# Kernel tuning notes

Measured on AMD Instinct MI355X. Metric: run time of the kernel, lower is better.

## Reference

```python
import jax, jax.numpy as jnp
import numpy as np

B, L, DW, DP = 128, 512, 256, 64
NF = 512          # num_filters == types == nr (forced by U.view / maxpool in source)
D = DW + 2 * DP   # 384
DWIN = 3 * D      # windowed feature width


def setup_inputs() -> dict:
    key = jax.random.key(0)
    ks = jax.random.split(key, 10)
    return {
        "x": jax.random.normal(ks[0], (B, L, DW), jnp.float32),
        "e1": jax.random.normal(ks[1], (B, DW), jnp.float32),
        "e2": jax.random.normal(ks[2], (B, DW), jnp.float32),
        "posVec": jax.random.normal(ks[3], (B, L, 2 * DP), jnp.float32),
        "We1": jax.random.normal(ks[4], (DW, DW), jnp.float32),
        "We2": jax.random.normal(ks[5], (DW, DW), jnp.float32),
        "U": jax.random.normal(ks[6], (NF, NF), jnp.float32),
        "conv_w": jax.random.normal(ks[7], (NF, DWIN), jnp.float32) * 0.02,
        "conv_b": jnp.zeros((NF,), jnp.float32),
        "rel_w": jax.random.normal(ks[8], (NF, NF), jnp.float32) * 0.02,  # y_embedding.weight (nr, num_filters)
    }


def reference(x, e1, e2, posVec, We1, We2, U, conv_w, conv_b, rel_w):
    # ---- input attention ----
    x_concat = jnp.concatenate([x, posVec], axis=-1)            # (B, L, D)
    px = jnp.pad(x_concat, ((0, 0), (1, 1), (0, 0)))            # pad seq by k=1
    w_concat = jnp.concatenate(
        [px[:, 0:L], px[:, 1:L + 1], px[:, 2:L + 2]], axis=-1)  # (B, L, 3D)
    A1 = jnp.einsum('bld,de,be->bl', x, We1, e1)                # (B, L)
    A2 = jnp.einsum('bld,de,be->bl', x, We2, e2)
    alpha = 0.5 * (jax.nn.softmax(A1, axis=1) + jax.nn.softmax(A2, axis=1))
    R = w_concat * alpha[:, :, None]                            # (B, L, 3D)
    # ---- convolution (kernel spans full window -> per-position linear) ----
    conv = jnp.tanh(jnp.einsum('bld,fd->bfl', R, conv_w) + conv_b[None, :, None])  # (B, F, L)
    # ---- attentive pooling ----
    G = jnp.einsum('bfl,ft,rt->blr', conv, U, rel_w)            # (B, L, nr)
    AP = jax.nn.softmax(G, axis=1)                              # softmax over seq positions
    wo = jnp.einsum('bfl,blr->bfr', conv, AP)                   # (B, F, nr)
    wo = jnp.max(wo, axis=2)                                    # MaxPool2d((1, types)) -> (B, F)
    wo = jax.nn.relu(wo)
    return wo, rel_w
```

## Files before the change

kernel.cpp:

```cpp
#include <hip/hip_runtime.h>
#include <hip/hip_bf16.h>

#define BB 128
#define LL 512
#define DW 256
#define DP 64
#define NF 512
#define DD 384
#define DWIN 1152
#define RR 512
#define LP 514

typedef __attribute__((ext_vector_type(8))) short short8;
typedef __attribute__((ext_vector_type(4))) short short4v;
typedef __attribute__((ext_vector_type(2))) short short2v;
typedef __attribute__((ext_vector_type(8))) _Float16 half8;
typedef __attribute__((ext_vector_type(4))) float f32x4;
typedef __attribute__((ext_vector_type(2))) float f32x2;

typedef __attribute__((address_space(1))) const void* gas_t;
typedef __attribute__((address_space(3))) void* las_t;

__device__ __forceinline__ void stage16(const void* g, void* l) {
    __builtin_amdgcn_global_load_lds((gas_t)g, (las_t)l, 16, 0, 0);
}

__device__ inline short f2h(float v) {
    _Float16 h = (_Float16)v;
    return *reinterpret_cast<short*>(&h);
}
__device__ inline int xcd_swz(int bid, int nwg) {
    return (bid & 7) * (nwg >> 3) + (bid >> 3);
}

__global__ void k_ve(const float* __restrict__ We1, const float* __restrict__ We2,
                     const float* __restrict__ e1, const float* __restrict__ e2,
                     float* __restrict__ v1, float* __restrict__ v2) {
    int b = blockIdx.x;
    int d = threadIdx.x;
    __shared__ float s1[DW], s2[DW];
    s1[d] = e1[b * DW + d];
    s2[d] = e2[b * DW + d];
    __syncthreads();
    float a1 = 0.f, a2 = 0.f;
    for (int e = 0; e < DW; ++e) {
        a1 += We1[d * DW + e] * s1[e];
        a2 += We2[d * DW + e] * s2[e];
    }
    v1[b * DW + d] = a1;
    v2[b * DW + d] = a2;
}

__global__ __launch_bounds__(256) void k_pack_logits(
    const float* __restrict__ x, const float* __restrict__ pv,
    const float* __restrict__ v1, const float* __restrict__ v2,
    short* __restrict__ pxp, float* __restrict__ A1, float* __restrict__ A2) {
    int gr = blockIdx.x * 4 + (threadIdx.x >> 6);
    int lane = threadIdx.x & 63;
    int b = gr / LP;
    int rr = gr - b * LP;
    short* dst = pxp + (size_t)gr * DD;
    if (rr == 0 || rr == LP - 1) {
        *(short4v*)(dst + lane * 4) = (short4v){0, 0, 0, 0};
        *(short2v*)(dst + 256 + lane * 2) = (short2v){0, 0};
        return;
    }
    int l = rr - 1;
    f32x4 xv = *(const f32x4*)(x + ((size_t)b * LL + l) * DW + lane * 4);
    f32x2 pvv = *(const f32x2*)(pv + ((size_t)b * LL + l) * (2 * DP) + lane * 2);
    f32x4 w1 = *(const f32x4*)(v1 + b * DW + lane * 4);
    f32x4 w2 = *(const f32x4*)(v2 + b * DW + lane * 4);
    float p1 = xv[0] * w1[0] + xv[1] * w1[1] + xv[2] * w1[2] + xv[3] * w1[3];
    float p2 = xv[0] * w2[0] + xv[1] * w2[1] + xv[2] * w2[2] + xv[3] * w2[3];
    for (int off = 32; off; off >>= 1) {
        p1 += __shfl_down(p1, off);
        p2 += __shfl_down(p2, off);
    }
    short4v ox;
#pragma unroll
    for (int j = 0; j < 4; ++j) ox[j] = f2h(xv[j]);
    *(short4v*)(dst + lane * 4) = ox;
    short2v op;
    op[0] = f2h(pvv[0]);
    op[1] = f2h(pvv[1]);
    *(short2v*)(dst + 256 + lane * 2) = op;
    if (lane == 0) { A1[b * LL + l] = p1; A2[b * LL + l] = p2; }
}

__global__ void k_alpha(const float* __restrict__ A1, const float* __restrict__ A2,
                        float* __restrict__ alpha) {
    int b = blockIdx.x;
    int l = threadIdx.x;
    __shared__ float s[LL];
    float a1 = A1[b * LL + l], a2 = A2[b * LL + l];

    s[l] = a1; __syncthreads();
    for (int st = 256; st; st >>= 1) { if (l < st) s[l] = fmaxf(s[l], s[l + st]); __syncthreads(); }
    float m1 = s[0]; __syncthreads();
    float e1x = expf(a1 - m1);
    s[l] = e1x; __syncthreads();
    for (int st = 256; st; st >>= 1) { if (l < st) s[l] += s[l + st]; __syncthreads(); }
    float d1 = s[0]; __syncthreads();

    s[l] = a2; __syncthreads();
    for (int st = 256; st; st >>= 1) { if (l < st) s[l] = fmaxf(s[l], s[l + st]); __syncthreads(); }
    float m2 = s[0]; __syncthreads();
    float e2x = expf(a2 - m2);
    s[l] = e2x; __syncthreads();
    for (int st = 256; st; st >>= 1) { if (l < st) s[l] += s[l + st]; __syncthreads(); }
    float d2 = s[0];

    alpha[b * LL + l] = 0.5f * (e1x / d1 + e2x / d2);
}

__global__ __launch_bounds__(256) void k_pack_w(const float* __restrict__ cw,
                                                short* __restrict__ cwb) {
    int idx = blockIdx.x * 256 + threadIdx.x;
    const float* src = cw + (size_t)idx * 8;
    f32x4 u0 = *(const f32x4*)(src);
    f32x4 u1 = *(const f32x4*)(src + 4);
    short8 v;
#pragma unroll
    for (int jj = 0; jj < 4; ++jj) { v[jj] = f2h(u0[jj]); v[jj + 4] = f2h(u1[jj]); }
    *(short8*)(cwb + (size_t)idx * 8) = v;
}

__global__ void k_w2t(const float* __restrict__ U, const float* __restrict__ relw,
                      short* __restrict__ Qf) {
    __shared__ float As[16][65], Bs[16][65];
    int r0 = blockIdx.y * 64, f0 = blockIdx.x * 64;
    int tid = threadIdx.x, ty = tid >> 4, tx = tid & 15;
    float acc[4][4] = {};
    for (int k0 = 0; k0 < NF; k0 += 16) {
        for (int i = 0; i < 4; ++i) {
            int lin = tid + 256 * i;
            int kk = lin & 15, mm = lin >> 4;
            As[kk][mm] = relw[(r0 + mm) * NF + k0 + kk];
            Bs[kk][mm] = U[(f0 + mm) * NF + k0 + kk];
        }
        __syncthreads();
        for (int kk = 0; kk < 16; ++kk) {
            float av[4], bv[4];
            for (int i = 0; i < 4; ++i) av[i] = As[kk][ty * 4 + i];
            for (int j = 0; j < 4; ++j) bv[j] = Bs[kk][tx * 4 + j];
            for (int i = 0; i < 4; ++i)
                for (int j = 0; j < 4; ++j) acc[i][j] += av[i] * bv[j];
        }
        __syncthreads();
    }
    for (int i = 0; i < 4; ++i)
        for (int j = 0; j < 4; ++j)
            Qf[(size_t)(r0 + ty * 4 + i) * NF + f0 + tx * 4 + j] = f2h(acc[i][j]);
}

__global__ __launch_bounds__(512, 2) void k_conv_mfma(
    const short* __restrict__ pxp, const short* __restrict__ cwb,
    const float* __restrict__ conv_b, const float* __restrict__ alpha,
    short* __restrict__ conv_lf, short* __restrict__ conv_fl) {
    int wg = xcd_swz(blockIdx.x, 512);
    int b = wg >> 2;
    int bl0 = ((wg >> 1) & 1) * 256;
    int bf0 = (wg & 1) * 256;
    int tid = threadIdx.x;
    int lane = tid & 63, w = tid >> 6;
    int wm = w >> 2, wn = w & 3;
    int lr = lane & 15, lg = lane >> 4;

    __shared__ __align__(16) char smem[131072];

    f32x4 acc[8][4];
#pragma unroll
    for (int i = 0; i < 8; ++i)
#pragma unroll
        for (int j = 0; j < 4; ++j) acc[i][j] = (f32x4){0.f, 0.f, 0.f, 0.f};

    int srow = lane >> 3;
    int sw = (lane & 7) ^ srow;
    const short* gA = pxp + ((size_t)b * LP + bl0 + w * 8 + srow) * DD + sw * 8;
    const short* gB = cwb + (size_t)(bf0 + w * 8 + srow) * DWIN + sw * 8;
    int p7 = lr & 7;

    {
        char* nb = smem;
#pragma unroll
        for (int c = 0; c < 4; ++c) {
            stage16(gA + (size_t)(64 * c) * DD, nb + (c * 64 + w * 8) * 128);
            stage16(gB + (size_t)(64 * c) * DWIN, nb + 32768 + (c * 64 + w * 8) * 128);
        }
    }
    __syncthreads();

    for (int kt = 0; kt < 18; ++kt) {
        const char* cb = smem + (kt & 1) * 65536;
        if (kt + 1 < 18) {
            char* nb = smem + ((kt + 1) & 1) * 65536;
            int k0 = (kt + 1) * 64;
#pragma unroll
            for (int c = 0; c < 4; ++c) {
                stage16(gA + (size_t)(64 * c) * DD + k0, nb + (c * 64 + w * 8) * 128);
                stage16(gB + (size_t)(64 * c) * DWIN + k0, nb + 32768 + (c * 64 + w * 8) * 128);
            }
        }
        half8 bf[4][2];
#pragma unroll
        for (int ni = 0; ni < 4; ++ni)
#pragma unroll
            for (int ks = 0; ks < 2; ++ks) {
                int cs = ks * 4 + lg;
                bf[ni][ks] = *(const half8*)(cb + 32768 +
                    (wn * 64 + ni * 16 + lr) * 128 + ((cs ^ p7) * 16));
            }
#pragma unroll
        for (int mh = 0; mh < 2; ++mh) {
            half8 af[4][2];
#pragma unroll
            for (int mi = 0; mi < 4; ++mi)
#pragma unroll
                for (int ks = 0; ks < 2; ++ks) {
                    int cs = ks * 4 + lg;
                    af[mi][ks] = *(const half8*)(cb +
                        (wm * 128 + mh * 64 + mi * 16 + lr) * 128 + ((cs ^ p7) * 16));
                }
            __builtin_amdgcn_s_setprio(1);
#pragma unroll
            for (int mi = 0; mi < 4; ++mi)
#pragma unroll
                for (int ni = 0; ni < 4; ++ni)
#pragma unroll
                    for (int ks = 0; ks < 2; ++ks)
                        acc[mh * 4 + mi][ni] = __builtin_amdgcn_mfma_f32_16x16x32_f16(
                            af[mi][ks], bf[ni][ks], acc[mh * 4 + mi][ni], 0, 0, 0);
            __builtin_amdgcn_s_setprio(0);
        }
        __syncthreads();
    }

    char* T = smem;
#pragma unroll
    for (int mi = 0; mi < 8; ++mi) {
        int lloc = wm * 128 + mi * 16 + lg * 4;
        int l = bl0 + lloc;
        f32x4 av = *(const f32x4*)(alpha + (size_t)b * LL + l);
#pragma unroll
        for (int ni = 0; ni < 4; ++ni) {
            int floc = wn * 64 + ni * 16 + lr;
            int f = bf0 + floc;
            float bias = conv_b[f];
            short4v o;
#pragma unroll
            for (int r = 0; r < 4; ++r) {
                float val = tanhf(av[r] * acc[mi][ni][r] + bias);
                short sv = f2h(val);
                o[r] = sv;
                conv_lf[((size_t)b * LL + l + r) * NF + f] = sv;
            }
            int c16 = lloc >> 3;
            *(short4v*)(T + floc * 512 + ((c16 ^ (floc & 31)) << 4) + (lloc & 7) * 2) = o;
        }
    }
    __syncthreads();
#pragma unroll
    for (int i = 0; i < 16; ++i) {
        int lin = tid + 512 * i;
        int frow = lin >> 5;
        int c16 = lin & 31;
        short8 v = *(const short8*)(T + frow * 512 + ((c16 ^ (frow & 31)) << 4));
        *(short8*)(conv_fl + ((size_t)b * NF + bf0 + frow) * LL + bl0 + c16 * 8) = v;
    }
}

__global__ __launch_bounds__(512) void k_g_mfma(
    const short* __restrict__ Qf,
    const short* __restrict__ convlf, _Float16* __restrict__ Gp) {
    const float LOG2E = 1.4426950408889634f;
    int wg = xcd_swz(blockIdx.x, 512);
    int b = wg >> 2;
    int r0 = (wg & 3) * 128;
    int tid = threadIdx.x, lane = tid & 63, w = tid >> 6;
    int wm = w >> 2, wn = w & 3;
    int lr = lane & 15, lg = lane >> 4;

    __shared__ __align__(16) char smem[81920];
    short* Ab = (short*)smem;
    short* Bb = (short*)(smem + 16384);
    float (*rowred)[4] = (float(*)[4])smem;

    f32x4 acc[4][8];
#pragma unroll
    for (int i = 0; i < 4; ++i)
#pragma unroll
        for (int j = 0; j < 8; ++j) acc[i][j] = (f32x4){0.f, 0.f, 0.f, 0.f};

    int trow = tid >> 3;
    int sw = (tid & 7) ^ (trow & 7);
    const short* gA = Qf + (size_t)(r0 + trow) * NF + sw * 8;
    const short* gB = convlf + (size_t)b * LL * NF + (size_t)trow * NF + sw * 8;
    short* lAd = Ab + w * 512;
    short* lBd = Bb + w * 512;
    int p7 = lr & 7;

    for (int kb = 0; kb < 8; ++kb) {
        int k0 = kb * 64;
#pragma unroll
        for (int c = 0; c < 2; ++c)
            stage16(gA + (size_t)(64 * c) * NF + k0, lAd + c * 4096);
#pragma unroll
        for (int c = 0; c < 8; ++c)
            stage16(gB + (size_t)(64 * c) * NF + k0, lBd + c * 4096);
        __syncthreads();
#pragma unroll
        for (int kk = 0; kk < 2; ++kk) {
            int cs = (kk << 2) + lg;
            half8 af[4], bf[8];
#pragma unroll
            for (int mi = 0; mi < 4; ++mi)
                af[mi] = *(const half8*)(Ab + (wm * 64 + mi * 16 + lr) * 64 + ((cs ^ p7) * 8));
#pragma unroll
            for (int ni = 0; ni < 8; ++ni)
                bf[ni] = *(const half8*)(Bb + (wn * 128 + ni * 16 + lr) * 64 + ((cs ^ p7) * 8));
#pragma unroll
            for (int mi = 0; mi < 4; ++mi)
#pragma unroll
                for (int ni = 0; ni < 8; ++ni)
                    acc[mi][ni] = __builtin_amdgcn_mfma_f32_16x16x32_f16(
                        af[mi], bf[ni], acc[mi][ni], 0, 0, 0);
        }
        __syncthreads();
    }

    float mrow[4][4];
#pragma unroll
    for (int mi = 0; mi < 4; ++mi)
#pragma unroll
        for (int rr = 0; rr < 4; ++rr) {
            float m = acc[mi][0][rr];
#pragma unroll
            for (int ni = 1; ni < 8; ++ni) m = fmaxf(m, acc[mi][ni][rr]);
            m = fmaxf(m, __shfl_xor(m, 1));
            m = fmaxf(m, __shfl_xor(m, 2));
            m = fmaxf(m, __shfl_xor(m, 4));
            m = fmaxf(m, __shfl_xor(m, 8));
            mrow[mi][rr] = m;
        }
    if (lr == 0) {
#pragma unroll
        for (int mi = 0; mi < 4; ++mi)
#pragma unroll
            for (int rr = 0; rr < 4; ++rr)
                rowred[wm * 64 + mi * 16 + lg * 4 + rr][wn] = mrow[mi][rr];
    }
    __syncthreads();
#pragma unroll
    for (int mi = 0; mi < 4; ++mi)
#pragma unroll
        for (int rr = 0; rr < 4; ++rr) {
            f32x4 rv = *(const f32x4*)rowred[wm * 64 + mi * 16 + lg * 4 + rr];
            mrow[mi][rr] = fmaxf(fmaxf(rv[0], rv[1]), fmaxf(rv[2], rv[3]));
        }
    __syncthreads();
    float srow[4][4];
#pragma unroll
    for (int mi = 0; mi < 4; ++mi)
#pragma unroll
        for (int rr = 0; rr < 4; ++rr) {
            float s = 0.f;
            float m = mrow[mi][rr];
#pragma unroll
            for (int ni = 0; ni < 8; ++ni) {
                float pp = exp2f((acc[mi][ni][rr] - m) * LOG2E);
                acc[mi][ni][rr] = pp;
                s += pp;
            }
            s += __shfl_xor(s, 1);
            s += __shfl_xor(s, 2);
            s += __shfl_xor(s, 4);
            s += __shfl_xor(s, 8);
            srow[mi][rr] = s;
        }
    if (lr == 0) {
#pragma unroll
        for (int mi = 0; mi < 4; ++mi)
#pragma unroll
            for (int rr = 0; rr < 4; ++rr)
                rowred[wm * 64 + mi * 16 + lg * 4 + rr][wn] = srow[mi][rr];
    }
    __syncthreads();
#pragma unroll
    for (int mi = 0; mi < 4; ++mi)
#pragma unroll
        for (int rr = 0; rr < 4; ++rr) {
            f32x4 rv = *(const f32x4*)rowred[wm * 64 + mi * 16 + lg * 4 + rr];
            srow[mi][rr] = 1.f / (rv[0] + rv[1] + rv[2] + rv[3]);
        }

#pragma unroll
    for (int mi = 0; mi < 4; ++mi)
#pragma unroll
        for (int ni = 0; ni < 8; ++ni)
#pragma unroll
            for (int rr = 0; rr < 4; ++rr) {
                int r = r0 + wm * 64 + mi * 16 + lg * 4 + rr;
                int l = wn * 128 + ni * 16 + lr;
                Gp[((size_t)b * RR + r) * LL + l] = (_Float16)(acc[mi][ni][rr] * srow[mi][rr]);
            }
}

__global__ __launch_bounds__(256) void k_wo_mfma(
    const short* __restrict__ convfl, const short* __restrict__ P,
    float* __restrict__ out) {
    int wg = xcd_swz(blockIdx.x, 2048);
    int b = wg >> 4;
    int f0 = ((wg >> 2) & 3) * 128;
    int r0 = (wg & 3) * 128;
    int tid = threadIdx.x, lane = tid & 63, w = tid >> 6;
    int wm = w >> 1, wn = w & 1;
    int lr = lane & 15, lg = lane >> 4;

    __shared__ __align__(16) char smem[65536];

    f32x4 acc[4][4];
    for (int i = 0; i < 4; ++i)
        for (int j = 0; j < 4; ++j) acc[i][j] = (f32x4){0.f, 0.f, 0.f, 0.f};

    int rowA = lane >> 3;
    int sw = (lane & 7) ^ rowA;
    const short* gA = convfl + (size_t)b * NF * LL + (size_t)(f0 + w * 32 + rowA) * LL + sw * 8;
    const short* gB = P + (size_t)b * RR * LL + (size_t)(r0 + w * 32 + rowA) * LL + sw * 8;
    int rA = wm * 64, rB = wn * 64;
    int p7 = lr & 7;

    {
        char* nbuf = smem;
#pragma unroll
        for (int c = 0; c < 4; ++c) {
            stage16(gA + (size_t)(8 * c) * LL, nbuf + w * 4096 + c * 1024);
            stage16(gB + (size_t)(8 * c) * LL, nbuf + 16384 + w * 4096 + c * 1024);
        }
    }

    for (int t = 0; t < 8; ++t) {
        char* cbuf = smem + (t & 1) * 32768;
        if (t + 1 < 8) {
            char* nbuf = smem + ((t + 1) & 1) * 32768;
            int k0 = (t + 1) * 64;
#pragma unroll
            for (int c = 0; c < 4; ++c) {
                stage16(gA + (size_t)(8 * c) * LL + k0, nbuf + w * 4096 + c * 1024);
                stage16(gB + (size_t)(8 * c) * LL + k0, nbuf + 16384 + w * 4096 + c * 1024);
            }
            asm volatile("s_waitcnt vmcnt(8)" ::: "memory");
        } else {
            asm volatile("s_waitcnt vmcnt(0)" ::: "memory");
        }
        __builtin_amdgcn_s_barrier();
        __builtin_amdgcn_sched_barrier(0);
        const short (*Ac)[64] = (const short(*)[64])cbuf;
        const short (*Bc)[64] = (const short(*)[64])(cbuf + 16384);
#pragma unroll
        for (int kk = 0; kk < 2; ++kk) {
            half8 af[4], bf[4];
            int cs = ((kk << 2) + lg);
#pragma unroll
            for (int mi = 0; mi < 4; ++mi)
                af[mi] = *(const half8*)(&Ac[rA + mi * 16 + lr][(cs ^ p7) * 8]);
#pragma unroll
            for (int ni = 0; ni < 4; ++ni)
                bf[ni] = *(const half8*)(&Bc[rB + ni * 16 + lr][(cs ^ p7) * 8]);
#pragma unroll
            for (int mi = 0; mi < 4; ++mi)
#pragma unroll
                for (int ni = 0; ni < 4; ++ni)
                    acc[mi][ni] = __builtin_amdgcn_mfma_f32_16x16x32_f16(
                        af[mi], bf[ni], acc[mi][ni], 0, 0, 0);
        }
        __builtin_amdgcn_sched_barrier(0);
        __builtin_amdgcn_s_barrier();
        __builtin_amdgcn_sched_barrier(0);
    }

    int fbase = f0 + wm * 64;
#pragma unroll
    for (int mi = 0; mi < 4; ++mi)
#pragma unroll
        for (int rr = 0; rr < 4; ++rr) {
            float m = acc[mi][0][rr];
#pragma unroll
            for (int ni = 1; ni < 4; ++ni) m = fmaxf(m, acc[mi][ni][rr]);
            m = fmaxf(m, __shfl_xor(m, 1));
            m = fmaxf(m, __shfl_xor(m, 2));
            m = fmaxf(m, __shfl_xor(m, 4));
            m = fmaxf(m, __shfl_xor(m, 8));
            if (lr == 0 && m > 0.f) {
                int f = fbase + mi * 16 + lg * 4 + rr;
                atomicMax((int*)&out[(size_t)b * NF + f], __float_as_int(m));
            }
        }
}

extern "C" void kernel_launch(void* const* d_in, const int* in_sizes, int n_in,
                              void* d_out, int out_size, void* d_ws, size_t ws_size,
                              hipStream_t stream) {
    const float* x      = (const float*)d_in[0];
    const float* e1     = (const float*)d_in[1];
    const float* e2     = (const float*)d_in[2];
    const float* posVec = (const float*)d_in[3];
    const float* We1    = (const float*)d_in[4];
    const float* We2    = (const float*)d_in[5];
    const float* U      = (const float*)d_in[6];
    const float* conv_w = (const float*)d_in[7];
    const float* conv_b = (const float*)d_in[8];
    const float* rel_w  = (const float*)d_in[9];
    float* out = (float*)d_out;

    char* p = (char*)d_ws;
    short* convlf = (short*)p;  p += (size_t)BB * LL * NF * 2;
    short* convfl = (short*)p;  p += (size_t)BB * NF * LL * 2;
    _Float16* Gp  = (_Float16*)p;  p += (size_t)BB * RR * LL * 2;
    short* pxp    = (short*)p;  p += (size_t)BB * LP * DD * 2;
    short* cwb    = (short*)p;  p += (size_t)NF * DWIN * 2;
    short* QfW    = (short*)p;  p += (size_t)RR * NF * 2;
    float* v1     = (float*)p;  p += (size_t)BB * DW * 4;
    float* v2     = (float*)p;  p += (size_t)BB * DW * 4;
    float* A1     = (float*)p;  p += (size_t)BB * LL * 4;
    float* A2     = (float*)p;  p += (size_t)BB * LL * 4;
    float* alpha  = (float*)p;  p += (size_t)BB * LL * 4;

    k_ve<<<BB, DW, 0, stream>>>(We1, We2, e1, e2, v1, v2);
    k_pack_logits<<<(BB * LP) / 4, 256, 0, stream>>>(x, posVec, v1, v2, pxp, A1, A2);
    k_alpha<<<BB, LL, 0, stream>>>(A1, A2, alpha);
    k_pack_w<<<(NF * DWIN / 8) / 256, 256, 0, stream>>>(conv_w, cwb);
    k_w2t<<<dim3(NF / 64, RR / 64), 256, 0, stream>>>(U, rel_w, QfW);
    k_conv_mfma<<<512, 512, 0, stream>>>(pxp, cwb, conv_b, alpha, convlf, convfl);
    k_g_mfma<<<512, 512, 0, stream>>>(QfW, convlf, Gp);
    hipMemsetAsync(d_out, 0, (size_t)BB * NF * sizeof(float), stream);
    k_wo_mfma<<<2048, 256, 0, stream>>>(convfl, (const short*)Gp, out);
    hipMemcpyAsync(out + BB * NF, rel_w, (size_t)NF * RR * sizeof(float),
                   hipMemcpyDeviceToDevice, stream);
}
```

Baseline: 315.5 us.

## Split conv GEMM K-loop into four phased sub-steps with finer-grained staging

Restructures the conv MFMA main loop into four phases per K tile. B and each half of A now have separate double buffers, and async global-to-LDS loads for the next tile are issued in chunks with explicit vmcnt waits and raw s_barrier instead of one full __syncthreads per tile. The A-row-to-wave mapping is permuted so each phase handles 32 rows per wave, and the epilogue index math is updated to match. The launch bound no longer requests two blocks per CU, which frees registers but may lower occupancy.

```diff
diff --git a/kernel.cpp b/kernel.cpp
--- a/kernel.cpp
+++ b/kernel.cpp
@@ -153,7 +153,7 @@
             Qf[(size_t)(r0 + ty * 4 + i) * NF + f0 + tx * 4 + j] = f2h(acc[i][j]);
 }
 
-__global__ __launch_bounds__(512, 2) void k_conv_mfma(
+__global__ __launch_bounds__(512) void k_conv_mfma(
     const short* __restrict__ pxp, const short* __restrict__ cwb,
     const float* __restrict__ conv_b, const float* __restrict__ alpha,
     short* __restrict__ conv_lf, short* __restrict__ conv_fl) {
@@ -174,71 +174,92 @@
 #pragma unroll
         for (int j = 0; j < 4; ++j) acc[i][j] = (f32x4){0.f, 0.f, 0.f, 0.f};
 
-    int srow = lane >> 3;
-    int sw = (lane & 7) ^ srow;
-    const short* gA = pxp + ((size_t)b * LP + bl0 + w * 8 + srow) * DD + sw * 8;
-    const short* gB = cwb + (size_t)(bf0 + w * 8 + srow) * DWIN + sw * 8;
+    int srow8 = w * 8 + (lane >> 3);
+    int swc = (lane & 7) ^ (srow8 & 7);
+    const short* gB = cwb + (size_t)(bf0 + srow8) * DWIN + swc * 8;
+    const short* gA = pxp + ((size_t)b * LP + bl0 + srow8) * DD + swc * 8;
     int p7 = lr & 7;
-
-    {
-        char* nb = smem;
-#pragma unroll
-        for (int c = 0; c < 4; ++c) {
-            stage16(gA + (size_t)(64 * c) * DD, nb + (c * 64 + w * 8) * 128);
-            stage16(gB + (size_t)(64 * c) * DWIN, nb + 32768 + (c * 64 + w * 8) * 128);
-        }
-    }
-    __syncthreads();
-
-    for (int kt = 0; kt < 18; ++kt) {
-        const char* cb = smem + (kt & 1) * 65536;
-        if (kt + 1 < 18) {
-            char* nb = smem + ((kt + 1) & 1) * 65536;
-            int k0 = (kt + 1) * 64;
-#pragma unroll
-            for (int c = 0; c < 4; ++c) {
-                stage16(gA + (size_t)(64 * c) * DD + k0, nb + (c * 64 + w * 8) * 128);
-                stage16(gB + (size_t)(64 * c) * DWIN + k0, nb + 32768 + (c * 64 + w * 8) * 128);
-            }
-        }
+    int ldst = w * 1024;
+
+#define STAGE_B(T) { char* d_ = smem + ((T) & 1) * 32768 + ldst; int k0_ = (T) * 64; \
+    stage16(gB + k0_, d_); \
+    stage16(gB + (size_t)64 * DWIN + k0_, d_ + 8192); \
+    stage16(gB + (size_t)128 * DWIN + k0_, d_ + 16384); \
+    stage16(gB + (size_t)192 * DWIN + k0_, d_ + 24576); }
+#define STAGE_A(T, half) { char* d_ = smem + 65536 + ((half) * 2 + ((T) & 1)) * 16384 + ldst; \
+    int k0_ = (T) * 64; \
+    stage16(gA + (size_t)((half) * 128) * DD + k0_, d_); \
+    stage16(gA + (size_t)((half) * 128 + 64) * DD + k0_, d_ + 8192); }
+
+    STAGE_B(0);
+    STAGE_A(0, 0);
+    STAGE_A(0, 1);
+
+    for (int T = 0; T < 18; ++T) {
+        int par = T & 1;
+        const char* Bb = smem + par * 32768;
         half8 bf[4][2];
 #pragma unroll
-        for (int ni = 0; ni < 4; ++ni)
-#pragma unroll
-            for (int ks = 0; ks < 2; ++ks) {
-                int cs = ks * 4 + lg;
-                bf[ni][ks] = *(const half8*)(cb + 32768 +
-                    (wn * 64 + ni * 16 + lr) * 128 + ((cs ^ p7) * 16));
-            }
-#pragma unroll
-        for (int mh = 0; mh < 2; ++mh) {
-            half8 af[4][2];
-#pragma unroll
-            for (int mi = 0; mi < 4; ++mi)
+        for (int p = 0; p < 4; ++p) {
+            if (p == 0) {
+                if (T + 1 < 18) {
+                    STAGE_B(T + 1);
+                    asm volatile("s_waitcnt vmcnt(6)" ::: "memory");
+                } else {
+                    asm volatile("s_waitcnt vmcnt(2)" ::: "memory");
+                }
+            } else if (p == 2) {
+                if (T + 1 < 18) {
+                    STAGE_A(T + 1, 0);
+                    asm volatile("s_waitcnt vmcnt(6)" ::: "memory");
+                } else {
+                    asm volatile("s_waitcnt vmcnt(0)" ::: "memory");
+                }
+            } else if (p == 3) {
+                if (T + 1 < 18) STAGE_A(T + 1, 1);
+            }
+            __builtin_amdgcn_s_barrier();
+            __builtin_amdgcn_sched_barrier(0);
+            if (p == 0) {
+#pragma unroll
+                for (int ni = 0; ni < 4; ++ni)
+#pragma unroll
+                    for (int ks = 0; ks < 2; ++ks) {
+                        int cs = ks * 4 + lg;
+                        bf[ni][ks] = *(const half8*)(Bb + (wn * 64 + ni * 16 + lr) * 128 + ((cs ^ p7) * 16));
+                    }
+            }
+            const char* Ab = smem + 65536 + ((p >> 1) * 2 + par) * 16384;
+            half8 af[2][2];
+#pragma unroll
+            for (int q = 0; q < 2; ++q)
 #pragma unroll
                 for (int ks = 0; ks < 2; ++ks) {
                     int cs = ks * 4 + lg;
-                    af[mi][ks] = *(const half8*)(cb +
-                        (wm * 128 + mh * 64 + mi * 16 + lr) * 128 + ((cs ^ p7) * 16));
+                    int R = (p & 1) * 64 + wm * 32 + q * 16 + lr;
+                    af[q][ks] = *(const half8*)(Ab + R * 128 + ((cs ^ p7) * 16));
                 }
             __builtin_amdgcn_s_setprio(1);
 #pragma unroll
-            for (int mi = 0; mi < 4; ++mi)
+            for (int q = 0; q < 2; ++q)
 #pragma unroll
                 for (int ni = 0; ni < 4; ++ni)
 #pragma unroll
                     for (int ks = 0; ks < 2; ++ks)
-                        acc[mh * 4 + mi][ni] = __builtin_amdgcn_mfma_f32_16x16x32_f16(
-                            af[mi][ks], bf[ni][ks], acc[mh * 4 + mi][ni], 0, 0, 0);
+                        acc[p * 2 + q][ni] = __builtin_amdgcn_mfma_f32_16x16x32_f16(
+                            af[q][ks], bf[ni][ks], acc[p * 2 + q][ni], 0, 0, 0);
             __builtin_amdgcn_s_setprio(0);
-        }
-        __syncthreads();
-    }
-
-    char* T = smem;
+            __builtin_amdgcn_sched_barrier(0);
+        }
+    }
+#undef STAGE_B
+#undef STAGE_A
+    __syncthreads();
+
+    char* T2 = smem;
 #pragma unroll
     for (int mi = 0; mi < 8; ++mi) {
-        int lloc = wm * 128 + mi * 16 + lg * 4;
+        int lloc = (mi >> 1) * 64 + wm * 32 + (mi & 1) * 16 + lg * 4;
         int l = bl0 + lloc;
         f32x4 av = *(const f32x4*)(alpha + (size_t)b * LL + l);
 #pragma unroll
@@ -255,7 +276,7 @@
                 conv_lf[((size_t)b * LL + l + r) * NF + f] = sv;
             }
             int c16 = lloc >> 3;
-            *(short4v*)(T + floc * 512 + ((c16 ^ (floc & 31)) << 4) + (lloc & 7) * 2) = o;
+            *(short4v*)(T2 + floc * 512 + ((c16 ^ (floc & 31)) << 4) + (lloc & 7) * 2) = o;
         }
     }
     __syncthreads();
@@ -264,7 +285,7 @@
         int lin = tid + 512 * i;
         int frow = lin >> 5;
         int c16 = lin & 31;
-        short8 v = *(const short8*)(T + frow * 512 + ((c16 ^ (frow & 31)) << 4));
+        short8 v = *(const short8*)(T2 + frow * 512 + ((c16 ^ (frow & 31)) << 4));
         *(short8*)(conv_fl + ((size_t)b * NF + bf0 + frow) * LL + bl0 + c16 * 8) = v;
     }
 }
```

Measured after the change: 318.5 us. Within noise of the previous version (+0.9%).
